# Kernel optimization log

Measured on AMD Instinct MI355X. Metric: run time of the kernel, lower is better.

Reference implementation:

```python
import jax, jax.numpy as jnp
import numpy as np

B, S, D = 4, 2048, 1024
H = 16
DH = D // H  # 64
DFF = 4096
EPS = 1e-5


def _layer_norm(x, g, b):
    mu = jnp.mean(x, axis=-1, keepdims=True)
    var = jnp.mean((x - mu) ** 2, axis=-1, keepdims=True)
    return (x - mu) * jax.lax.rsqrt(var + EPS) * g + b


def _rope(x):
    # x: [B, S, H, DH]; same rotation for every head (module reuses one RoPE).
    inv_freq = 1.0 / (10000.0 ** (jnp.arange(0, DH, 2, dtype=jnp.float32) / DH))
    pos = jnp.arange(S, dtype=jnp.float32)
    freqs = pos[:, None] * inv_freq[None, :]            # [S, DH/2]
    cos = jnp.cos(freqs)[None, :, None, :]              # [1, S, 1, DH/2]
    sin = jnp.sin(freqs)[None, :, None, :]
    x_even = x[..., 0::2]
    x_odd = x[..., 1::2]
    r_even = x_even * cos - x_odd * sin
    r_odd = x_even * sin + x_odd * cos
    return jnp.stack([r_even, r_odd], axis=-1).reshape(x.shape)


def setup_inputs() -> dict:
    key = jax.random.key(0)
    ks = jax.random.split(key, 10)
    s_d = 1.0 / np.sqrt(D)
    s_f = 1.0 / np.sqrt(DFF)
    return {
        "x": jax.random.normal(ks[0], (B, S, D), jnp.float32),
        "Wq": jax.random.uniform(ks[1], (D, D), jnp.float32, -s_d, s_d),
        "bq": jnp.zeros((D,), jnp.float32),
        "Wk": jax.random.uniform(ks[2], (D, D), jnp.float32, -s_d, s_d),
        "bk": jnp.zeros((D,), jnp.float32),
        "Wv": jax.random.uniform(ks[3], (D, D), jnp.float32, -s_d, s_d),
        "bv": jnp.zeros((D,), jnp.float32),
        "Wo": jax.random.uniform(ks[4], (D, D), jnp.float32, -s_d, s_d),
        "bo": jnp.zeros((D,), jnp.float32),
        "W1": jax.random.uniform(ks[5], (DFF, D), jnp.float32, -s_d, s_d),
        "bf1": jnp.zeros((DFF,), jnp.float32),
        "W2": jax.random.uniform(ks[6], (D, DFF), jnp.float32, -s_f, s_f),
        "bf2": jnp.zeros((D,), jnp.float32),
        "g1": jnp.ones((D,), jnp.float32),
        "be1": jnp.zeros((D,), jnp.float32),
        "g2": jnp.ones((D,), jnp.float32),
        "be2": jnp.zeros((D,), jnp.float32),
    }


def reference(x, Wq, bq, Wk, bk, Wv, bv, Wo, bo, W1, bf1, W2, bf2, g1, be1, g2, be2):
    # Pre-LN self-attention block (dropout is identity at eval)
    residual = x
    h = _layer_norm(x, g1, be1)
    q = (h @ Wq.T + bq).reshape(B, S, H, DH)
    k = (h @ Wk.T + bk).reshape(B, S, H, DH)
    v = (h @ Wv.T + bv).reshape(B, S, H, DH)
    q = _rope(q)
    k = _rope(k)
    # scores: [B, H, Sq, Sk]
    scores = jnp.einsum("bqhd,bkhd->bhqk", q, k) / np.sqrt(DH)
    causal = jnp.tril(jnp.ones((S, S), dtype=bool))
    scores = jnp.where(causal[None, None], scores, -jnp.inf)
    attn = jax.nn.softmax(scores, axis=-1)
    out = jnp.einsum("bhqk,bkhd->bqhd", attn, v).reshape(B, S, D)
    out = out @ Wo.T + bo
    x = residual + out
    # FFN block
    residual = x
    h = _layer_norm(x, g2, be2)
    ff = jax.nn.relu(h @ W1.T + bf1) @ W2.T + bf2
    return residual + ff
```

## Files before the change

kernel.cpp:

```cpp
#include <hip/hip_runtime.h>

typedef __attribute__((ext_vector_type(8))) short bh8;
typedef __attribute__((ext_vector_type(4))) short sh4;
typedef __attribute__((ext_vector_type(4))) float f4;
typedef __attribute__((ext_vector_type(16))) float f16v;
typedef __attribute__((ext_vector_type(4))) unsigned int u4;

__device__ __forceinline__ unsigned short f2bf(float x) {
  unsigned int u = __float_as_uint(x);
  u += 0x7fffu + ((u >> 16) & 1u);
  return (unsigned short)(u >> 16);
}
__device__ __forceinline__ float bf2f(short x) {
  return __uint_as_float(((unsigned int)(unsigned short)x) << 16);
}
__device__ __forceinline__ unsigned cvtpk_bf16(float lo, float hi) {
  unsigned r;
  asm("v_cvt_pk_bf16_f32 %0, %1, %2" : "=v"(r) : "v"(lo), "v"(hi));
  return r;
}
__device__ __forceinline__ void gl_lds16(const short* g, short* l) {
  __builtin_amdgcn_global_load_lds(
      (const __attribute__((address_space(1))) unsigned int*)g,
      (__attribute__((address_space(3))) unsigned int*)l, 16, 0, 0);
}

#define VM4() asm volatile("s_waitcnt vmcnt(4)" ::: "memory")
#define VM2() asm volatile("s_waitcnt vmcnt(2)" ::: "memory")
#define VM0() asm volatile("s_waitcnt vmcnt(0)" ::: "memory")

__global__ __launch_bounds__(256)
void rope_table(float* __restrict__ ct, float* __restrict__ st) {
  const int idx = blockIdx.x * 256 + threadIdx.x;
  const int s = idx >> 5, j = idx & 31;
  const float invf = expf(-0.28782313662425574f * (float)j);
  const float f = (float)s * invf;
  ct[idx] = cosf(f);
  st[idx] = sinf(f);
}

__global__ __launch_bounds__(256)
void concat_bias(const float* __restrict__ bq, const float* __restrict__ bk,
                 const float* __restrict__ bv, float* __restrict__ bqkv) {
  const int i = blockIdx.x * 256 + threadIdx.x;
  bqkv[i] = (i < 1024) ? bq[i] : ((i < 2048) ? bk[i - 1024] : bv[i - 2048]);
}

__global__ __launch_bounds__(256)
void w2bf_all(const float* __restrict__ Wq, const float* __restrict__ Wk,
              const float* __restrict__ Wv, const float* __restrict__ Wo,
              const float* __restrict__ W1, const float* __restrict__ W2,
              short* __restrict__ wqkvb, short* __restrict__ wob,
              short* __restrict__ w1b, short* __restrict__ w2b) {
  const int which = blockIdx.y;
  const float* src; short* dst; int n;
  switch (which) {
    case 0: src = Wq; dst = wqkvb;                 n = 1 << 20; break;
    case 1: src = Wk; dst = wqkvb + (1 << 20);     n = 1 << 20; break;
    case 2: src = Wv; dst = wqkvb + (2 << 20);     n = 1 << 20; break;
    case 3: src = Wo; dst = wob;                   n = 1 << 20; break;
    case 4: src = W1; dst = w1b;                   n = 1 << 22; break;
    default: src = W2; dst = w2b;                  n = 1 << 22; break;
  }
  const int i = (blockIdx.x * 256 + threadIdx.x) * 4;
  if (i >= n) return;
  f4 v = *(const f4*)(src + i);
#pragma unroll
  for (int j = 0; j < 4; ++j) dst[i + j] = (short)f2bf(v[j]);
}

__global__ __launch_bounds__(256)
void layernorm_bf(const float* __restrict__ x, const float* __restrict__ g,
                  const float* __restrict__ be, short* __restrict__ out) {
  __shared__ float sb[4];
  const int row = blockIdx.x, t = threadIdx.x;
  const float* xr = x + (size_t)row * 1024;
  f4 v = *(const f4*)(xr + t * 4);
  float s = v[0] + v[1] + v[2] + v[3];
#pragma unroll
  for (int mk = 1; mk < 64; mk <<= 1) s += __shfl_xor(s, mk, 64);
  if ((t & 63) == 0) sb[t >> 6] = s;
  __syncthreads();
  const float mean = (sb[0] + sb[1] + sb[2] + sb[3]) * (1.0f / 1024.0f);
  __syncthreads();
  f4 d;
#pragma unroll
  for (int i = 0; i < 4; ++i) d[i] = v[i] - mean;
  float s2 = d[0] * d[0] + d[1] * d[1] + d[2] * d[2] + d[3] * d[3];
#pragma unroll
  for (int mk = 1; mk < 64; mk <<= 1) s2 += __shfl_xor(s2, mk, 64);
  if ((t & 63) == 0) sb[t >> 6] = s2;
  __syncthreads();
  const float var = (sb[0] + sb[1] + sb[2] + sb[3]) * (1.0f / 1024.0f);
  const float rstd = rsqrtf(var + 1e-5f);
  const f4 gg = *(const f4*)(g + t * 4);
  const f4 bb = *(const f4*)(be + t * 4);
#pragma unroll
  for (int i = 0; i < 4; ++i)
    out[(size_t)row * 1024 + t * 4 + i] = (short)f2bf(d[i] * rstd * gg[i] + bb[i]);
}

__global__ __launch_bounds__(256)
void rope_apply(short* __restrict__ qkv, const float* __restrict__ ct,
                const float* __restrict__ st) {
  const int off = blockIdx.y ? 1024 : 0;
  const int gid = blockIdx.x * 256 + threadIdx.x;
  const int row = gid >> 7, chn = gid & 127;
  const int srow = row & 2047;
  const int col = chn * 8;
  const int j0 = (col & 63) >> 1;
  short* p = qkv + (size_t)row * 3072 + off + col;
  bh8 vv = *(const bh8*)p;
  bh8 r;
#pragma unroll
  for (int pp = 0; pp < 4; ++pp) {
    const float e = bf2f(vv[2 * pp]), od = bf2f(vv[2 * pp + 1]);
    const float c = ct[srow * 32 + j0 + pp], sn = st[srow * 32 + j0 + pp];
    r[2 * pp]     = (short)f2bf(e * c - od * sn);
    r[2 * pp + 1] = (short)f2bf(e * sn + od * c);
  }
  *(bh8*)p = r;
}

#define STG(dst, gbase, kt, half)                                              \
  {                                                                            \
    _Pragma("unroll") for (int cc = 0; cc < 2; ++cc) {                         \
      const int rr = (half) * 128 + cc * 64 + sr;                              \
      gl_lds16(gbase + (size_t)rr * K + (kt) * 64 + ssl * 8,                   \
               &dst[rr * 64 + (t & 7) * 8]);                                   \
    }                                                                          \
  }

#define PHASE(bf, q, STAGE_STMT, VMSTMT)                                       \
  {                                                                            \
    if ((q) == 0) {                                                            \
      _Pragma("unroll") for (int ni = 0; ni < 4; ++ni)                         \
      _Pragma("unroll") for (int kk = 0; kk < 2; ++kk)                         \
        bfrag[ni][kk] = *(const bh8*)(&Bs[bf][(wn * 64 + ni * 16 + (lane & 15)) * 64 + (((lane >> 4) + kk * 4) ^ (lane & 7)) * 8]); \
    }                                                                          \
    _Pragma("unroll") for (int j = 0; j < 2; ++j)                              \
    _Pragma("unroll") for (int kk = 0; kk < 2; ++kk)                           \
      af[j][kk] = *(const bh8*)(&As[bf][(wm * MROWS + (2 * (q) + j) * 16 + (lane & 15)) * 64 + (((lane >> 4) + kk * 4) ^ (lane & 7)) * 8]); \
    STAGE_STMT;                                                                \
    __builtin_amdgcn_s_barrier();                                              \
    asm volatile("s_waitcnt lgkmcnt(0)" ::: "memory");                         \
    __builtin_amdgcn_sched_barrier(0);                                         \
    __builtin_amdgcn_s_setprio(1);                                             \
    _Pragma("unroll") for (int j = 0; j < 2; ++j)                              \
    _Pragma("unroll") for (int ni = 0; ni < 4; ++ni)                           \
    _Pragma("unroll") for (int kk = 0; kk < 2; ++kk)                           \
      acc[2 * (q) + j][ni] = __builtin_amdgcn_mfma_f32_16x16x32_bf16(          \
          af[j][kk], bfrag[ni][kk], acc[2 * (q) + j][ni], 0, 0, 0);            \
    __builtin_amdgcn_s_setprio(0);                                             \
    VMSTMT;                                                                    \
    __builtin_amdgcn_s_barrier();                                              \
  }

template <int BM, int RELU, int OBF16, int VOUT>
__global__ __launch_bounds__(512, 2)
void gemm256(const short* __restrict__ A, const short* __restrict__ Bw,
             const float* __restrict__ bias,
             short* __restrict__ Vt,
             short* __restrict__ Cb, float* __restrict__ Cf,
             int M, int N, int K) {
  constexpr int MROWS = BM / 2;
  __shared__ short As[2][BM * 64];
  __shared__ short Bs[2][256 * 64];
  const int t = threadIdx.x, lane = t & 63;
  const int w = t >> 6, wm = w >> 2, wn = w & 3;
  const int nwg = gridDim.x, cpx = nwg >> 3;
  int flat = blockIdx.x;
  flat = (flat & 7) * cpx + (flat >> 3);
  const int nbn = N >> 8;
  const int bn = flat % nbn, bm = flat / nbn;
  const short* Ab = A + (size_t)(bm * BM) * K;
  const short* Bb = Bw + (size_t)(bn * 256) * K;
  const int nkt = K >> 6;
  const int sr = t >> 3;
  const int ssl = (t & 7) ^ (sr & 7);
  f4 acc[BM / 32][4] = {};
  bh8 bfrag[4][2], af[2][2];

  STG(Bs[0], Bb, 0, 0); STG(Bs[0], Bb, 0, 1);
  STG(As[0], Ab, 0, 0); if (BM == 256) STG(As[0], Ab, 0, 1);
  STG(Bs[1], Bb, 1, 0); STG(Bs[1], Bb, 1, 1);
  VM4();
  __builtin_amdgcn_s_barrier();

  if (BM == 256) {
    for (int i2 = 0; i2 < nkt; i2 += 2) {
      const bool nf = (i2 + 2 < nkt);
      PHASE(0, 0, STG(As[1], Ab, i2 + 1, 0), );
      PHASE(0, 1, STG(As[1], Ab, i2 + 1, 1), );
      PHASE(0, 2, if (nf) STG(Bs[0], Bb, i2 + 2, 0), );
      PHASE(0, 3, if (nf) STG(Bs[0], Bb, i2 + 2, 1),
            if (nf) { VM4(); } else { VM0(); });
      PHASE(1, 0, if (nf) STG(As[0], Ab, i2 + 2, 0), );
      PHASE(1, 1, if (nf) STG(As[0], Ab, i2 + 2, 1), );
      PHASE(1, 2, if (nf) STG(Bs[1], Bb, i2 + 3, 0), );
      PHASE(1, 3, if (nf) STG(Bs[1], Bb, i2 + 3, 1), if (nf) { VM4(); });
    }
  } else {
    for (int i2 = 0; i2 < nkt; i2 += 2) {
      const bool nf = (i2 + 2 < nkt);
      PHASE(0, 0, STG(As[1], Ab, i2 + 1, 0), );
      PHASE(0, 1, if (nf) { STG(Bs[0], Bb, i2 + 2, 0); STG(Bs[0], Bb, i2 + 2, 1); },
            if (nf) { VM4(); } else { VM0(); });
      PHASE(1, 0, if (nf) STG(As[0], Ab, i2 + 2, 0), );
      PHASE(1, 1, if (nf) { STG(Bs[1], Bb, i2 + 3, 0); STG(Bs[1], Bb, i2 + 3, 1); },
            if (nf) { VM4(); });
    }
  }

  const int rb = bm * BM + wm * MROWS + ((lane >> 4) << 2);
  const int cb = bn * 256 + wn * 64 + (lane & 15);
  if (VOUT && bn >= 8) {
#pragma unroll
    for (int mi = 0; mi < BM / 32; ++mi) {
#pragma unroll
      for (int ni = 0; ni < 4; ++ni) {
        const int c = cb + ni * 16;
        const float bi = bias[c];
        const int hh = (c - 2048) >> 6, dd = (c - 2048) & 63;
        const int r0 = rb + mi * 16;
        const int bb2 = r0 >> 11, ss = r0 & 2047;
        sh4 pk;
#pragma unroll
        for (int jr = 0; jr < 4; ++jr) pk[jr] = (short)f2bf(acc[mi][ni][jr] + bi);
        *(sh4*)(Vt + ((size_t)(bb2 * 16 + hh) * 64 + dd) * 2048 + ss) = pk;
      }
    }
  } else {
#pragma unroll
    for (int mi = 0; mi < BM / 32; ++mi) {
#pragma unroll
      for (int ni = 0; ni < 4; ++ni) {
        const int c = cb + ni * 16;
        const float bi = bias[c];
#pragma unroll
        for (int jr = 0; jr < 4; ++jr) {
          const int r = rb + mi * 16 + jr;
          float v = acc[mi][ni][jr] + bi;
          if (RELU) v = fmaxf(v, 0.f);
          if (OBF16) Cb[(size_t)r * N + c] = (short)f2bf(v);
          else       Cf[(size_t)r * N + c] = v;
        }
      }
    }
  }
}

#define PH64(bf, q, STAGE_STMT, VMSTMT)                                        \
  {                                                                            \
    if ((q) == 0) {                                                            \
      _Pragma("unroll") for (int ni = 0; ni < 2; ++ni)                         \
      _Pragma("unroll") for (int kk = 0; kk < 2; ++kk)                         \
        bfrag[ni][kk] = *(const bh8*)(&Bs[bf][(wn * 32 + ni * 16 + (lane & 15)) * 64 + (((lane >> 4) + kk * 4) ^ (lane & 7)) * 8]); \
    }                                                                          \
    _Pragma("unroll") for (int j = 0; j < 2; ++j)                              \
    _Pragma("unroll") for (int kk = 0; kk < 2; ++kk)                           \
      af[j][kk] = *(const bh8*)(&As[bf][(wm * 64 + (2 * (q) + j) * 16 + (lane & 15)) * 64 + (((lane >> 4) + kk * 4) ^ (lane & 7)) * 8]); \
    STAGE_STMT;                                                                \
    __builtin_amdgcn_s_barrier();                                              \
    asm volatile("s_waitcnt lgkmcnt(0)" ::: "memory");                         \
    __builtin_amdgcn_sched_barrier(0);                                         \
    __builtin_amdgcn_s_setprio(1);                                             \
    _Pragma("unroll") for (int j = 0; j < 2; ++j)                              \
    _Pragma("unroll") for (int ni = 0; ni < 2; ++ni)                           \
    _Pragma("unroll") for (int kk = 0; kk < 2; ++kk)                           \
      acc[2 * (q) + j][ni] = __builtin_amdgcn_mfma_f32_16x16x32_bf16(          \
          af[j][kk], bfrag[ni][kk], acc[2 * (q) + j][ni], 0, 0, 0);            \
    __builtin_amdgcn_s_setprio(0);                                             \
    VMSTMT;                                                                    \
    __builtin_amdgcn_s_barrier();                                              \
  }

template <int RELU, int RES, int OBF16>
__global__ __launch_bounds__(512, 4)
void gemm_bn128(const short* __restrict__ A, const short* __restrict__ Bw,
                const float* __restrict__ bias, const float* __restrict__ res,
                short* __restrict__ Cb, float* __restrict__ Cf,
                int M, int N, int K) {
  __shared__ short As[2][128 * 64];
  __shared__ short Bs[2][128 * 64];
  const int t = threadIdx.x, lane = t & 63;
  const int w = t >> 6, wm = w >> 2, wn = w & 3;
  const int nwg = gridDim.x, cpx = nwg >> 3;
  int flat = blockIdx.x;
  flat = (flat & 7) * cpx + (flat >> 3);
  const int nbn = N >> 7;
  const int bn = flat % nbn, bm = flat / nbn;
  const short* Ab = A + (size_t)(bm * 128) * K;
  const short* Bb = Bw + (size_t)(bn * 128) * K;
  const int nkt = K >> 6;
  const int sr = t >> 3;
  const int ssl = (t & 7) ^ (sr & 7);
  f4 acc[4][2] = {};
  bh8 bfrag[2][2], af[2][2];

  STG(Bs[0], Bb, 0, 0); STG(As[0], Ab, 0, 0);
  STG(Bs[1], Bb, 1, 0);
  VM2();
  __builtin_amdgcn_s_barrier();

  for (int i2 = 0; i2 < nkt; i2 += 2) {
    const bool nf = (i2 + 2 < nkt);
    PH64(0, 0, STG(As[1], Ab, i2 + 1, 0), );
    PH64(0, 1, if (nf) STG(Bs[0], Bb, i2 + 2, 0),
         if (nf) { VM2(); } else { VM0(); });
    PH64(1, 0, if (nf) STG(As[0], Ab, i2 + 2, 0), );
    PH64(1, 1, if (nf) STG(Bs[1], Bb, i2 + 3, 0), if (nf) { VM2(); });
  }

  const int rb = bm * 128 + wm * 64 + ((lane >> 4) << 2);
  const int cb = bn * 128 + wn * 32 + (lane & 15);
#pragma unroll
  for (int mi = 0; mi < 4; ++mi) {
#pragma unroll
    for (int ni = 0; ni < 2; ++ni) {
      const int c = cb + ni * 16;
      const float bi = bias[c];
#pragma unroll
      for (int jr = 0; jr < 4; ++jr) {
        const int r = rb + mi * 16 + jr;
        float v = acc[mi][ni][jr] + bi;
        if (RES) v += res[(size_t)r * N + c];
        if (RELU) v = fmaxf(v, 0.f);
        if (OBF16) Cb[(size_t)r * N + c] = (short)f2bf(v);
        else       Cf[(size_t)r * N + c] = v;
      }
    }
  }
}

__global__ __launch_bounds__(512, 4)
void flash_attn(const short* __restrict__ qkv, const short* __restrict__ vt,
                short* __restrict__ o) {
  __shared__ short lds[2 * 2 * 64 * 72];
  const int t = threadIdx.x, lane = t & 63, w = t >> 6;
  const int l31 = lane & 31, l5 = lane >> 5;
  const int id = blockIdx.x;
  const int half = id >> 8, j = id & 255;
  const int xcd = j & 7, y = j >> 3;
  const int bh = xcd * 8 + (y >> 2);
  const int pr = y & 3;
  const int qt = half ? pr : 7 - pr;
  const int b = bh >> 4, hh = bh & 15;
  const int r8 = t >> 3, c8 = (t & 7) * 8;
  const float NEG_INF = -__builtin_inff();

  const short* kbase = qkv + (size_t)b * 2048 * 3072 + 1024 + hh * 64;
  const short* vbase = vt + ((size_t)bh * 64 + r8) * 2048;
  const int wq0 = qt * 256 + w * 32;
  const int nt = 4 * qt + 4;

  bh8 qf[4];
  {
    const short* qrow = qkv + ((size_t)b * 2048 + wq0 + l31) * 3072 + hh * 64 + l5 * 8;
#pragma unroll
    for (int dk = 0; dk < 4; ++dk) qf[dk] = *(const bh8*)(qrow + dk * 16);
  }
  f16v o0 = {}, o1 = {};
  float mr = NEG_INF, lsum = 0.f;

  {
    bh8 rk = *(const bh8*)(kbase + (size_t)r8 * 3072 + c8);
    bh8 rv = *(const bh8*)(vbase + c8);
    *(bh8*)(&lds[r8 * 72 + c8]) = rk;
    *(bh8*)(&lds[4608 + r8 * 72 + c8]) = rv;
  }

  for (int kt = 0; kt < nt; ++kt) {
    __syncthreads();
    const int cur = kt & 1, nxt = cur ^ 1;
    bh8 rk, rv;
    const bool more = (kt + 1 < nt);
    if (more) {
      rk = *(const bh8*)(kbase + (size_t)((kt + 1) * 64 + r8) * 3072 + c8);
      rv = *(const bh8*)(vbase + (kt + 1) * 64 + c8);
    }
    const int kvb = kt * 64;
    if (kvb <= wq0 + 31) {
      const short* Kl = &lds[cur * 9216];
      const short* Vl = &lds[cur * 9216 + 4608];
      f16v s0 = {}, s1 = {};
#pragma unroll
      for (int dk = 0; dk < 4; ++dk) {
        bh8 ka0 = *(const bh8*)(&Kl[l31 * 72 + dk * 16 + l5 * 8]);
        bh8 ka1 = *(const bh8*)(&Kl[(32 + l31) * 72 + dk * 16 + l5 * 8]);
        s0 = __builtin_amdgcn_mfma_f32_32x32x16_bf16(ka0, qf[dk], s0, 0, 0, 0);
        s1 = __builtin_amdgcn_mfma_f32_32x32x16_bf16(ka1, qf[dk], s1, 0, 0, 0);
      }
      if (kvb + 63 > wq0) {
        const int qq = wq0 + l31;
        const int kvo = kvb + l5 * 4;
#pragma unroll
        for (int r = 0; r < 16; ++r) {
          const int kv0 = kvo + (r & 3) + 8 * (r >> 2);
          if (kv0 > qq) s0[r] = NEG_INF;
          if (kv0 + 32 > qq) s1[r] = NEG_INF;
        }
      }
      float mx = s0[0];
#pragma unroll
      for (int r = 1; r < 16; ++r) mx = fmaxf(mx, s0[r]);
#pragma unroll
      for (int r = 0; r < 16; ++r) mx = fmaxf(mx, s1[r]);
      mx = fmaxf(mx, __shfl_xor(mx, 32, 64));
      const bool keep = __all(mx <= mr + 8.0f);
      float mn, al;
      if (keep) { mn = mr; al = 1.0f; }
      else {
        mn = fmaxf(mr, mx);
        al = __expf((mr - mn) * 0.125f);
        mr = mn;
      }
      float rsA = 0.f, rsB = 0.f;
#pragma unroll
      for (int r = 0; r < 16; ++r) {
        const float p0 = __expf((s0[r] - mn) * 0.125f);
        const float p1 = __expf((s1[r] - mn) * 0.125f);
        s0[r] = p0; s1[r] = p1;
        rsA += p0; rsB += p1;
      }
      float rs = rsA + rsB;
      rs += __shfl_xor(rs, 32, 64);
      if (keep) {
        lsum += rs;
      } else {
        lsum = lsum * al + rs;
#pragma unroll
        for (int r = 0; r < 16; ++r) { o0[r] *= al; o1[r] *= al; }
      }
      float pp[32];
#pragma unroll
      for (int r = 0; r < 16; ++r) { pp[r] = s0[r]; pp[16 + r] = s1[r]; }
      const bool lo32 = (l5 == 0);
#pragma unroll
      for (int ks = 0; ks < 4; ++ks) {
        const int base = (ks >> 1) * 16 + (ks & 1) * 8;
        const unsigned e0 = cvtpk_bf16(pp[base + 0], pp[base + 1]);
        const unsigned e1 = cvtpk_bf16(pp[base + 2], pp[base + 3]);
        const unsigned q0 = cvtpk_bf16(pp[base + 4], pp[base + 5]);
        const unsigned q1 = cvtpk_bf16(pp[base + 6], pp[base + 7]);
        const unsigned sel0 = lo32 ? q0 : e0;
        const unsigned sel1 = lo32 ? q1 : e1;
        const unsigned rx0 = (unsigned)__shfl_xor((int)sel0, 32, 64);
        const unsigned rx1 = (unsigned)__shfl_xor((int)sel1, 32, 64);
        u4 frag;
        frag[0] = lo32 ? e0 : rx0;
        frag[1] = lo32 ? e1 : rx1;
        frag[2] = lo32 ? rx0 : q0;
        frag[3] = lo32 ? rx1 : q1;
        const bh8 pb = *(const bh8*)&frag;
        bh8 va0 = *(const bh8*)(&Vl[l31 * 72 + ks * 16 + l5 * 8]);
        bh8 va1 = *(const bh8*)(&Vl[(32 + l31) * 72 + ks * 16 + l5 * 8]);
        o0 = __builtin_amdgcn_mfma_f32_32x32x16_bf16(va0, pb, o0, 0, 0, 0);
        o1 = __builtin_amdgcn_mfma_f32_32x32x16_bf16(va1, pb, o1, 0, 0, 0);
      }
    }
    if (more) {
      *(bh8*)(&lds[nxt * 9216 + r8 * 72 + c8]) = rk;
      *(bh8*)(&lds[nxt * 9216 + 4608 + r8 * 72 + c8]) = rv;
    }
  }

  const float inv = 1.0f / lsum;
  __syncthreads();
  short* Ot = lds;
#pragma unroll
  for (int r = 0; r < 16; ++r) {
    const int d = (r & 3) + 8 * (r >> 2) + 4 * l5;
    Ot[(w * 32 + l31) * 72 + d]      = (short)f2bf(o0[r] * inv);
    Ot[(w * 32 + l31) * 72 + 32 + d] = (short)f2bf(o1[r] * inv);
  }
  __syncthreads();
  const int qrow = t >> 1, hf = t & 1;
  short* orow = o + ((size_t)b * 2048 + qt * 256 + qrow) * 1024 + hh * 64 + hf * 32;
#pragma unroll
  for (int i = 0; i < 4; ++i)
    *(bh8*)(orow + i * 8) = *(const bh8*)(&Ot[qrow * 72 + hf * 32 + i * 8]);
}

extern "C" void kernel_launch(void* const* d_in, const int* in_sizes, int n_in,
                              void* d_out, int out_size, void* d_ws, size_t ws_size,
                              hipStream_t stream) {
  const float* x   = (const float*)d_in[0];
  const float* Wq  = (const float*)d_in[1];
  const float* bq  = (const float*)d_in[2];
  const float* Wk  = (const float*)d_in[3];
  const float* bk  = (const float*)d_in[4];
  const float* Wv  = (const float*)d_in[5];
  const float* bv  = (const float*)d_in[6];
  const float* Wo  = (const float*)d_in[7];
  const float* bo  = (const float*)d_in[8];
  const float* W1  = (const float*)d_in[9];
  const float* bf1 = (const float*)d_in[10];
  const float* W2  = (const float*)d_in[11];
  const float* bf2 = (const float*)d_in[12];
  const float* g1  = (const float*)d_in[13];
  const float* be1 = (const float*)d_in[14];
  const float* g2  = (const float*)d_in[15];
  const float* be2 = (const float*)d_in[16];
  float* out = (float*)d_out;

  char* ws = (char*)d_ws;
  const size_t MB = 1u << 20;
  short* h_ob  = (short*)ws;
  short* qkv   = (short*)(ws + 16 * MB);
  short* f1    = (short*)(ws + 16 * MB);
  short* vtb   = (short*)(ws + 64 * MB);
  short* wqkvb = (short*)(ws + 80 * MB);
  short* wob   = (short*)(ws + 86 * MB);
  short* w1b   = (short*)(ws + 88 * MB);
  short* w2b   = (short*)(ws + 96 * MB);
  float* ct    = (float*)(ws + 104 * MB);
  float* st    = ct + 65536;
  float* bqkv  = st + 65536;
  float* x2    = out;

  rope_table<<<256, 256, 0, stream>>>(ct, st);
  concat_bias<<<12, 256, 0, stream>>>(bq, bk, bv, bqkv);
  w2bf_all<<<dim3(4096, 6), 256, 0, stream>>>(Wq, Wk, Wv, Wo, W1, W2,
                                              wqkvb, wob, w1b, w2b);

  layernorm_bf<<<8192, 256, 0, stream>>>(x, g1, be1, h_ob);

  gemm256<128, 0, 1, 1><<<768, 512, 0, stream>>>(h_ob, wqkvb, bqkv, vtb, qkv, nullptr, 8192, 3072, 1024);

  rope_apply<<<dim3(4096, 2), 256, 0, stream>>>(qkv, ct, st);

  flash_attn<<<512, 512, 0, stream>>>(qkv, vtb, h_ob);

  gemm_bn128<0, 1, 0><<<512, 512, 0, stream>>>(h_ob, wob, bo, x, nullptr, x2, 8192, 1024, 1024);

  layernorm_bf<<<8192, 256, 0, stream>>>(x2, g2, be2, h_ob);

  gemm256<256, 1, 1, 0><<<512, 512, 0, stream>>>(h_ob, w1b, bf1, nullptr, f1, nullptr, 8192, 4096, 1024);

  gemm_bn128<0, 1, 0><<<512, 512, 0, stream>>>(f1, w2b, bf2, x2, nullptr, out, 8192, 1024, 4096);
}
```

Baseline: 361.3 us.

## Fuse RoPE into QKV GEMM epilogue and use 128x128 tiles for all GEMMs

Removes the separate rope_apply kernel by applying the rotary embedding inside the QKV GEMM epilogue, pairing even and odd columns with a lane shuffle. This saves a full read and write pass over Q and K. It also drops the 256-wide gemm256 kernel and runs both the QKV and FFN1 GEMMs on the 128x128 gemm_bn128 kernel with more workgroups. The smaller tiles give less data reuse per tile and more global traffic, in exchange for higher occupancy and one less launch.

```diff
diff --git a/kernel.cpp b/kernel.cpp
--- a/kernel.cpp
+++ b/kernel.cpp
@@ -25,7 +25,6 @@
       (__attribute__((address_space(3))) unsigned int*)l, 16, 0, 0);
 }
 
-#define VM4() asm volatile("s_waitcnt vmcnt(4)" ::: "memory")
 #define VM2() asm volatile("s_waitcnt vmcnt(2)" ::: "memory")
 #define VM0() asm volatile("s_waitcnt vmcnt(0)" ::: "memory")
 
@@ -100,28 +99,6 @@
     out[(size_t)row * 1024 + t * 4 + i] = (short)f2bf(d[i] * rstd * gg[i] + bb[i]);
 }
 
-__global__ __launch_bounds__(256)
-void rope_apply(short* __restrict__ qkv, const float* __restrict__ ct,
-                const float* __restrict__ st) {
-  const int off = blockIdx.y ? 1024 : 0;
-  const int gid = blockIdx.x * 256 + threadIdx.x;
-  const int row = gid >> 7, chn = gid & 127;
-  const int srow = row & 2047;
-  const int col = chn * 8;
-  const int j0 = (col & 63) >> 1;
-  short* p = qkv + (size_t)row * 3072 + off + col;
-  bh8 vv = *(const bh8*)p;
-  bh8 r;
-#pragma unroll
-  for (int pp = 0; pp < 4; ++pp) {
-    const float e = bf2f(vv[2 * pp]), od = bf2f(vv[2 * pp + 1]);
-    const float c = ct[srow * 32 + j0 + pp], sn = st[srow * 32 + j0 + pp];
-    r[2 * pp]     = (short)f2bf(e * c - od * sn);
-    r[2 * pp + 1] = (short)f2bf(e * sn + od * c);
-  }
-  *(bh8*)p = r;
-}
-
 #define STG(dst, gbase, kt, half)                                              \
   {                                                                            \
     _Pragma("unroll") for (int cc = 0; cc < 2; ++cc) {                         \
@@ -130,125 +107,6 @@
                &dst[rr * 64 + (t & 7) * 8]);                                   \
     }                                                                          \
   }
-
-#define PHASE(bf, q, STAGE_STMT, VMSTMT)                                       \
-  {                                                                            \
-    if ((q) == 0) {                                                            \
-      _Pragma("unroll") for (int ni = 0; ni < 4; ++ni)                         \
-      _Pragma("unroll") for (int kk = 0; kk < 2; ++kk)                         \
-        bfrag[ni][kk] = *(const bh8*)(&Bs[bf][(wn * 64 + ni * 16 + (lane & 15)) * 64 + (((lane >> 4) + kk * 4) ^ (lane & 7)) * 8]); \
-    }                                                                          \
-    _Pragma("unroll") for (int j = 0; j < 2; ++j)                              \
-    _Pragma("unroll") for (int kk = 0; kk < 2; ++kk)                           \
-      af[j][kk] = *(const bh8*)(&As[bf][(wm * MROWS + (2 * (q) + j) * 16 + (lane & 15)) * 64 + (((lane >> 4) + kk * 4) ^ (lane & 7)) * 8]); \
-    STAGE_STMT;                                                                \
-    __builtin_amdgcn_s_barrier();                                              \
-    asm volatile("s_waitcnt lgkmcnt(0)" ::: "memory");                         \
-    __builtin_amdgcn_sched_barrier(0);                                         \
-    __builtin_amdgcn_s_setprio(1);                                             \
-    _Pragma("unroll") for (int j = 0; j < 2; ++j)                              \
-    _Pragma("unroll") for (int ni = 0; ni < 4; ++ni)                           \
-    _Pragma("unroll") for (int kk = 0; kk < 2; ++kk)                           \
-      acc[2 * (q) + j][ni] = __builtin_amdgcn_mfma_f32_16x16x32_bf16(          \
-          af[j][kk], bfrag[ni][kk], acc[2 * (q) + j][ni], 0, 0, 0);            \
-    __builtin_amdgcn_s_setprio(0);                                             \
-    VMSTMT;                                                                    \
-    __builtin_amdgcn_s_barrier();                                              \
-  }
-
-template <int BM, int RELU, int OBF16, int VOUT>
-__global__ __launch_bounds__(512, 2)
-void gemm256(const short* __restrict__ A, const short* __restrict__ Bw,
-             const float* __restrict__ bias,
-             short* __restrict__ Vt,
-             short* __restrict__ Cb, float* __restrict__ Cf,
-             int M, int N, int K) {
-  constexpr int MROWS = BM / 2;
-  __shared__ short As[2][BM * 64];
-  __shared__ short Bs[2][256 * 64];
-  const int t = threadIdx.x, lane = t & 63;
-  const int w = t >> 6, wm = w >> 2, wn = w & 3;
-  const int nwg = gridDim.x, cpx = nwg >> 3;
-  int flat = blockIdx.x;
-  flat = (flat & 7) * cpx + (flat >> 3);
-  const int nbn = N >> 8;
-  const int bn = flat % nbn, bm = flat / nbn;
-  const short* Ab = A + (size_t)(bm * BM) * K;
-  const short* Bb = Bw + (size_t)(bn * 256) * K;
-  const int nkt = K >> 6;
-  const int sr = t >> 3;
-  const int ssl = (t & 7) ^ (sr & 7);
-  f4 acc[BM / 32][4] = {};
-  bh8 bfrag[4][2], af[2][2];
-
-  STG(Bs[0], Bb, 0, 0); STG(Bs[0], Bb, 0, 1);
-  STG(As[0], Ab, 0, 0); if (BM == 256) STG(As[0], Ab, 0, 1);
-  STG(Bs[1], Bb, 1, 0); STG(Bs[1], Bb, 1, 1);
-  VM4();
-  __builtin_amdgcn_s_barrier();
-
-  if (BM == 256) {
-    for (int i2 = 0; i2 < nkt; i2 += 2) {
-      const bool nf = (i2 + 2 < nkt);
-      PHASE(0, 0, STG(As[1], Ab, i2 + 1, 0), );
-      PHASE(0, 1, STG(As[1], Ab, i2 + 1, 1), );
-      PHASE(0, 2, if (nf) STG(Bs[0], Bb, i2 + 2, 0), );
-      PHASE(0, 3, if (nf) STG(Bs[0], Bb, i2 + 2, 1),
-            if (nf) { VM4(); } else { VM0(); });
-      PHASE(1, 0, if (nf) STG(As[0], Ab, i2 + 2, 0), );
-      PHASE(1, 1, if (nf) STG(As[0], Ab, i2 + 2, 1), );
-      PHASE(1, 2, if (nf) STG(Bs[1], Bb, i2 + 3, 0), );
-      PHASE(1, 3, if (nf) STG(Bs[1], Bb, i2 + 3, 1), if (nf) { VM4(); });
-    }
-  } else {
-    for (int i2 = 0; i2 < nkt; i2 += 2) {
-      const bool nf = (i2 + 2 < nkt);
-      PHASE(0, 0, STG(As[1], Ab, i2 + 1, 0), );
-      PHASE(0, 1, if (nf) { STG(Bs[0], Bb, i2 + 2, 0); STG(Bs[0], Bb, i2 + 2, 1); },
-            if (nf) { VM4(); } else { VM0(); });
-      PHASE(1, 0, if (nf) STG(As[0], Ab, i2 + 2, 0), );
-      PHASE(1, 1, if (nf) { STG(Bs[1], Bb, i2 + 3, 0); STG(Bs[1], Bb, i2 + 3, 1); },
-            if (nf) { VM4(); });
-    }
-  }
-
-  const int rb = bm * BM + wm * MROWS + ((lane >> 4) << 2);
-  const int cb = bn * 256 + wn * 64 + (lane & 15);
-  if (VOUT && bn >= 8) {
-#pragma unroll
-    for (int mi = 0; mi < BM / 32; ++mi) {
-#pragma unroll
-      for (int ni = 0; ni < 4; ++ni) {
-        const int c = cb + ni * 16;
-        const float bi = bias[c];
-        const int hh = (c - 2048) >> 6, dd = (c - 2048) & 63;
-        const int r0 = rb + mi * 16;
-        const int bb2 = r0 >> 11, ss = r0 & 2047;
-        sh4 pk;
-#pragma unroll
-        for (int jr = 0; jr < 4; ++jr) pk[jr] = (short)f2bf(acc[mi][ni][jr] + bi);
-        *(sh4*)(Vt + ((size_t)(bb2 * 16 + hh) * 64 + dd) * 2048 + ss) = pk;
-      }
-    }
-  } else {
-#pragma unroll
-    for (int mi = 0; mi < BM / 32; ++mi) {
-#pragma unroll
-      for (int ni = 0; ni < 4; ++ni) {
-        const int c = cb + ni * 16;
-        const float bi = bias[c];
-#pragma unroll
-        for (int jr = 0; jr < 4; ++jr) {
-          const int r = rb + mi * 16 + jr;
-          float v = acc[mi][ni][jr] + bi;
-          if (RELU) v = fmaxf(v, 0.f);
-          if (OBF16) Cb[(size_t)r * N + c] = (short)f2bf(v);
-          else       Cf[(size_t)r * N + c] = v;
-        }
-      }
-    }
-  }
-}
 
 #define PH64(bf, q, STAGE_STMT, VMSTMT)                                        \
   {                                                                            \
@@ -275,10 +133,12 @@
     __builtin_amdgcn_s_barrier();                                              \
   }
 
-template <int RELU, int RES, int OBF16>
+template <int RELU, int RES, int OBF16, int QKVMODE>
 __global__ __launch_bounds__(512, 4)
 void gemm_bn128(const short* __restrict__ A, const short* __restrict__ Bw,
                 const float* __restrict__ bias, const float* __restrict__ res,
+                const float* __restrict__ ct, const float* __restrict__ st,
+                short* __restrict__ Vt,
                 short* __restrict__ Cb, float* __restrict__ Cf,
                 int M, int N, int K) {
   __shared__ short As[2][128 * 64];
@@ -314,20 +174,59 @@
 
   const int rb = bm * 128 + wm * 64 + ((lane >> 4) << 2);
   const int cb = bn * 128 + wn * 32 + (lane & 15);
-#pragma unroll
-  for (int mi = 0; mi < 4; ++mi) {
-#pragma unroll
-    for (int ni = 0; ni < 2; ++ni) {
-      const int c = cb + ni * 16;
-      const float bi = bias[c];
-#pragma unroll
-      for (int jr = 0; jr < 4; ++jr) {
-        const int r = rb + mi * 16 + jr;
-        float v = acc[mi][ni][jr] + bi;
-        if (RES) v += res[(size_t)r * N + c];
-        if (RELU) v = fmaxf(v, 0.f);
-        if (OBF16) Cb[(size_t)r * N + c] = (short)f2bf(v);
-        else       Cf[(size_t)r * N + c] = v;
+  if (QKVMODE && bn >= 16) {
+#pragma unroll
+    for (int mi = 0; mi < 4; ++mi) {
+#pragma unroll
+      for (int ni = 0; ni < 2; ++ni) {
+        const int c = cb + ni * 16;
+        const float bi = bias[c];
+        const int hh = (c - 2048) >> 6, dd = (c - 2048) & 63;
+        const int r0 = rb + mi * 16;
+        const int bb2 = r0 >> 11, ss = r0 & 2047;
+        sh4 pk;
+#pragma unroll
+        for (int jr = 0; jr < 4; ++jr) pk[jr] = (short)f2bf(acc[mi][ni][jr] + bi);
+        *(sh4*)(Vt + ((size_t)(bb2 * 16 + hh) * 64 + dd) * 2048 + ss) = pk;
+      }
+    }
+  } else if (QKVMODE) {
+    const bool evenc = (lane & 1) == 0;
+#pragma unroll
+    for (int mi = 0; mi < 4; ++mi) {
+#pragma unroll
+      for (int ni = 0; ni < 2; ++ni) {
+        const int c = cb + ni * 16;
+        const float bi = bias[c];
+        const int j0 = (c & 63) >> 1;
+#pragma unroll
+        for (int jr = 0; jr < 4; ++jr) {
+          const int r = rb + mi * 16 + jr;
+          const int s = r & 2047;
+          const float v = acc[mi][ni][jr] + bi;
+          const float pv = __shfl_xor(v, 1, 64);
+          const float cs = ct[s * 32 + j0], sn = st[s * 32 + j0];
+          const float o = evenc ? (v * cs - pv * sn) : (pv * sn + v * cs);
+          Cb[(size_t)r * N + c] = (short)f2bf(o);
+        }
+      }
+    }
+  } else {
+#pragma unroll
+    for (int mi = 0; mi < 4; ++mi) {
+#pragma unroll
+      for (int ni = 0; ni < 2; ++ni) {
+        const int c = cb + ni * 16;
+        const float bi = bias[c];
+#pragma unroll
+        for (int jr = 0; jr < 4; ++jr) {
+          const int r = rb + mi * 16 + jr;
+          float v = acc[mi][ni][jr] + bi;
+          if (RES) v += res[(size_t)r * N + c];
+          if (RELU) v = fmaxf(v, 0.f);
+          if (OBF16) Cb[(size_t)r * N + c] = (short)f2bf(v);
+          else       Cf[(size_t)r * N + c] = v;
+        }
       }
     }
   }
@@ -526,17 +425,23 @@
 
   layernorm_bf<<<8192, 256, 0, stream>>>(x, g1, be1, h_ob);
 
-  gemm256<128, 0, 1, 1><<<768, 512, 0, stream>>>(h_ob, wqkvb, bqkv, vtb, qkv, nullptr, 8192, 3072, 1024);
-
-  rope_apply<<<dim3(4096, 2), 256, 0, stream>>>(qkv, ct, st);
+  gemm_bn128<0, 0, 1, 1><<<1536, 512, 0, stream>>>(h_ob, wqkvb, bqkv, nullptr,
+                                                   ct, st, vtb, qkv, nullptr,
+                                                   8192, 3072, 1024);
 
   flash_attn<<<512, 512, 0, stream>>>(qkv, vtb, h_ob);
 
-  gemm_bn128<0, 1, 0><<<512, 512, 0, stream>>>(h_ob, wob, bo, x, nullptr, x2, 8192, 1024, 1024);
+  gemm_bn128<0, 1, 0, 0><<<512, 512, 0, stream>>>(h_ob, wob, bo, x,
+                                                  nullptr, nullptr, nullptr,
+                                                  nullptr, x2, 8192, 1024, 1024);
 
   layernorm_bf<<<8192, 256, 0, stream>>>(x2, g2, be2, h_ob);
 
-  gemm256<256, 1, 1, 0><<<512, 512, 0, stream>>>(h_ob, w1b, bf1, nullptr, f1, nullptr, 8192, 4096, 1024);
-
-  gemm_bn128<0, 1, 0><<<512, 512, 0, stream>>>(f1, w2b, bf2, x2, nullptr, out, 8192, 1024, 4096);
-}
+  gemm_bn128<1, 0, 1, 0><<<2048, 512, 0, stream>>>(h_ob, w1b, bf1, nullptr,
+                                                   nullptr, nullptr, nullptr,
+                                                   f1, nullptr, 8192, 4096, 1024);
+
+  gemm_bn128<0, 1, 0, 0><<<512, 512, 0, stream>>>(f1, w2b, bf2, x2,
+                                                  nullptr, nullptr, nullptr,
+                                                  nullptr, out, 8192, 1024, 4096);
+}
```

Measured after the change: 360.1 us. Within noise of the previous version (-0.4%).
